# Kernel tuning notes

Measured on AMD Instinct MI355X. Metric: run time of the kernel, lower is better.

## Reference

```python
import jax, jax.numpy as jnp
import numpy as np

B, S, D, H, HD = 4, 2048, 768, 12, 64


def setup_inputs() -> dict:
    key = jax.random.key(0)
    ks = jax.random.split(key, 9)
    s = 1.0 / np.sqrt(D)
    return {
        "hidden_state": jax.random.normal(ks[0], (B, S, D), jnp.float32),
        "Wq": jax.random.normal(ks[1], (H, D, HD), jnp.float32) * s,
        "bq": jax.random.normal(ks[2], (H, HD), jnp.float32) * 0.02,
        "Wk": jax.random.normal(ks[3], (H, D, HD), jnp.float32) * s,
        "bk": jax.random.normal(ks[4], (H, HD), jnp.float32) * 0.02,
        "Wv": jax.random.normal(ks[5], (H, D, HD), jnp.float32) * s,
        "bv": jax.random.normal(ks[6], (H, HD), jnp.float32) * 0.02,
        "Wo": jax.random.normal(ks[7], (D, D), jnp.float32) * s,
        "bo": jax.random.normal(ks[8], (D,), jnp.float32) * 0.02,
    }


def reference(hidden_state, Wq, bq, Wk, bk, Wv, bv, Wo, bo):
    # per-head projections, batched over heads: [B,H,S,HD]
    q = jnp.einsum("bsd,hde->bhse", hidden_state, Wq) + bq[None, :, None, :]
    k = jnp.einsum("bsd,hde->bhse", hidden_state, Wk) + bk[None, :, None, :]
    v = jnp.einsum("bsd,hde->bhse", hidden_state, Wv) + bv[None, :, None, :]
    scale = 1.0 / jnp.sqrt(jnp.asarray(HD, q.dtype))
    scores = jnp.einsum("bhse,bhte->bhst", q, k) * scale  # [B,H,S,S]
    attn = jax.nn.softmax(scores, axis=-1)
    out = jnp.einsum("bhst,bhte->bhse", attn, v)  # [B,H,S,HD]
    # concat heads in head order -> [B,S,D]
    out = out.transpose(0, 2, 1, 3).reshape(B, S, D)
    return out @ Wo.T + bo
```

## Files before the change

### kernel.cpp

```cpp
#include <hip/hip_runtime.h>
#include <hip/hip_bf16.h>

typedef unsigned short u16;
typedef __attribute__((ext_vector_type(8))) short short8;
typedef __attribute__((ext_vector_type(4))) float f32x4;

#define B_ 4
#define S_ 2048
#define D_ 768
#define H_ 12
#define HD_ 64

__device__ __forceinline__ u16 f2bf(float f) {
  union { float f; unsigned u; } c; c.f = f;
  unsigned u = c.u;
  unsigned lsb = (u >> 16) & 1u;
  u += 0x7fffu + lsb;
  return (u16)(u >> 16);
}

__global__ __launch_bounds__(256) void k_cvt_x(const float* __restrict__ x,
                                               u16* __restrict__ xb, int n4) {
  int i = blockIdx.x * 256 + threadIdx.x;
  if (i < n4) {
    float4 v = reinterpret_cast<const float4*>(x)[i];
    ushort4 o;
    o.x = f2bf(v.x); o.y = f2bf(v.y); o.z = f2bf(v.z); o.w = f2bf(v.w);
    reinterpret_cast<ushort4*>(xb)[i] = o;
  }
}

__global__ __launch_bounds__(256) void k_repack_w(const float* __restrict__ Wq,
                                                  const float* __restrict__ Wk,
                                                  const float* __restrict__ Wv,
                                                  const float* __restrict__ Wo,
                                                  u16* __restrict__ Wt,
                                                  u16* __restrict__ Wob) {
  int idx = blockIdx.x * 256 + threadIdx.x;
  const int WSZ = D_ * D_;
  if (idx < 3 * WSZ) {
    int t = idx / WSZ, r = idx % WSZ;
    int n = r / D_, d = r % D_;
    int h = n >> 6, e = n & 63;
    const float* W = (t == 0) ? Wq : (t == 1) ? Wk : Wv;
    Wt[idx] = f2bf(W[h * (D_ * HD_) + d * HD_ + e]);
  } else {
    int o = idx - 3 * WSZ;
    if (o < WSZ) Wob[o] = f2bf(Wo[o]);
  }
}

__global__ __launch_bounds__(256) void k_gemm_qkv(const u16* __restrict__ Xb,
                                                  const u16* __restrict__ Wt,
                                                  const float* __restrict__ bq,
                                                  const float* __restrict__ bk,
                                                  u16* __restrict__ Qw,
                                                  u16* __restrict__ Kw) {
  const int t = blockIdx.z;
  const u16* Bmat = Wt + t * (D_ * D_);
  const float* bias = (t == 0) ? bq : bk;
  u16* Out = (t == 0) ? Qw : Kw;
  const float scale = (t == 0) ? 0.125f : 1.0f;
  const int m0 = blockIdx.x * 128, n0 = blockIdx.y * 128;
  __shared__ __align__(16) u16 Al[128][40];
  __shared__ __align__(16) u16 Bl[128][40];
  const int tid = threadIdx.x;
  const int lane = tid & 63, w = tid >> 6;
  const int wm = (w >> 1) * 64, wn = (w & 1) * 64;
  const int lg = lane >> 4, lr = lane & 15;
  f32x4 acc[4][4] = {};
  for (int k0 = 0; k0 < D_; k0 += 32) {
    __syncthreads();
#pragma unroll
    for (int rep = 0; rep < 2; ++rep) {
      int item = tid + rep * 256;
      int row = item >> 2, ch = (item & 3) * 8;
      uint4 av = *reinterpret_cast<const uint4*>(&Xb[(m0 + row) * D_ + k0 + ch]);
      *reinterpret_cast<uint4*>(&Al[row][ch]) = av;
      uint4 bv2 = *reinterpret_cast<const uint4*>(&Bmat[(n0 + row) * D_ + k0 + ch]);
      *reinterpret_cast<uint4*>(&Bl[row][ch]) = bv2;
    }
    __syncthreads();
    short8 af[4], bf[4];
#pragma unroll
    for (int i = 0; i < 4; i++)
      af[i] = *reinterpret_cast<const short8*>(&Al[wm + i * 16 + lr][lg * 8]);
#pragma unroll
    for (int i = 0; i < 4; i++)
      bf[i] = *reinterpret_cast<const short8*>(&Bl[wn + i * 16 + lr][lg * 8]);
#pragma unroll
    for (int mi = 0; mi < 4; mi++)
#pragma unroll
      for (int ni = 0; ni < 4; ni++)
        acc[mi][ni] = __builtin_amdgcn_mfma_f32_16x16x32_bf16(af[mi], bf[ni], acc[mi][ni], 0, 0, 0);
  }
#pragma unroll
  for (int ni = 0; ni < 4; ni++) {
    int n = n0 + wn + ni * 16 + lr;
    float bn = bias[n];
    int h = n >> 6, e = n & 63;
#pragma unroll
    for (int mi = 0; mi < 4; mi++) {
#pragma unroll
      for (int r = 0; r < 4; r++) {
        int m = m0 + wm + mi * 16 + lg * 4 + r;
        int b = m >> 11, s = m & 2047;
        float v = (acc[mi][ni][r] + bn) * scale;
        Out[((b * H_ + h) * S_ + s) * HD_ + e] = f2bf(v);
      }
    }
  }
}

__global__ __launch_bounds__(256) void k_gemm_v(const u16* __restrict__ Xb,
                                                const u16* __restrict__ Wt,
                                                const float* __restrict__ bv,
                                                u16* __restrict__ VwT) {
  const u16* Bmat = Wt + 2 * (D_ * D_);
  const int m0 = blockIdx.x * 128, n0 = blockIdx.y * 128;
  __shared__ __align__(16) u16 Al[128][40];
  __shared__ __align__(16) u16 Bl[128][40];
  const int tid = threadIdx.x;
  const int lane = tid & 63, w = tid >> 6;
  const int wm = (w >> 1) * 64, wn = (w & 1) * 64;
  const int lg = lane >> 4, lr = lane & 15;
  f32x4 acc[4][4] = {};
  for (int k0 = 0; k0 < D_; k0 += 32) {
    __syncthreads();
#pragma unroll
    for (int rep = 0; rep < 2; ++rep) {
      int item = tid + rep * 256;
      int row = item >> 2, ch = (item & 3) * 8;
      uint4 av = *reinterpret_cast<const uint4*>(&Xb[(m0 + row) * D_ + k0 + ch]);
      *reinterpret_cast<uint4*>(&Al[row][ch]) = av;
      uint4 bv2 = *reinterpret_cast<const uint4*>(&Bmat[(n0 + row) * D_ + k0 + ch]);
      *reinterpret_cast<uint4*>(&Bl[row][ch]) = bv2;
    }
    __syncthreads();
    short8 af[4], bf[4];
#pragma unroll
    for (int i = 0; i < 4; i++)
      af[i] = *reinterpret_cast<const short8*>(&Al[wm + i * 16 + lr][lg * 8]);
#pragma unroll
    for (int i = 0; i < 4; i++)
      bf[i] = *reinterpret_cast<const short8*>(&Bl[wn + i * 16 + lr][lg * 8]);
#pragma unroll
    for (int ni = 0; ni < 4; ni++)
#pragma unroll
      for (int mi = 0; mi < 4; mi++)
        acc[ni][mi] = __builtin_amdgcn_mfma_f32_16x16x32_bf16(bf[ni], af[mi], acc[ni][mi], 0, 0, 0);
  }
#pragma unroll
  for (int ni = 0; ni < 4; ni++) {
#pragma unroll
    for (int r = 0; r < 4; r++) {
      int n = n0 + wn + ni * 16 + lg * 4 + r;
      int h = n >> 6, e = n & 63;
      float bn = bv[n];
#pragma unroll
      for (int mi = 0; mi < 4; mi++) {
        int m = m0 + wm + mi * 16 + lr;
        int b = m >> 11, s = m & 2047;
        VwT[((b * H_ + h) * HD_ + e) * S_ + s] = f2bf(acc[ni][mi][r] + bn);
      }
    }
  }
}

__global__ __launch_bounds__(256) void k_attn(const u16* __restrict__ Qw,
                                              const u16* __restrict__ Kw,
                                              const u16* __restrict__ VwT,
                                              u16* __restrict__ An) {
  const int qb = blockIdx.x;
  const int bh = blockIdx.y;
  const int b = bh / H_, h = bh % H_;
  const int tid = threadIdx.x, lane = tid & 63, w = tid >> 6;
  const int lg = lane >> 4, lr = lane & 15;
  __shared__ __align__(16) u16 Kl[64][72];
  __shared__ __align__(16) u16 Vt[64][72];
  __shared__ __align__(16) u16 Pb[4][32][72];
  const u16* Qp = Qw + (bh * S_ + qb * 128 + w * 32) * HD_;
  const u16* Kp = Kw + bh * S_ * HD_;
  const u16* VTp = VwT + bh * HD_ * S_;
  const int srow0 = tid >> 3, srow1 = (tid + 256) >> 3;
  const int sch = (tid & 7) * 8;
  short8 qf[2][2];
#pragma unroll
  for (int qif = 0; qif < 2; qif++)
#pragma unroll
    for (int es = 0; es < 2; es++)
      qf[qif][es] = *reinterpret_cast<const short8*>(&Qp[(qif * 16 + lr) * HD_ + es * 32 + lg * 8]);
  f32x4 acc[2][4] = {};
  float mcol[2] = {-INFINITY, -INFINITY};
  float lcol[2] = {0.f, 0.f};

  {
    uint4 k0a = *reinterpret_cast<const uint4*>(&Kp[srow0 * HD_ + sch]);
    uint4 k0b = *reinterpret_cast<const uint4*>(&Kp[srow1 * HD_ + sch]);
    uint4 v0a = *reinterpret_cast<const uint4*>(&VTp[srow0 * S_ + sch]);
    uint4 v0b = *reinterpret_cast<const uint4*>(&VTp[srow1 * S_ + sch]);
    *reinterpret_cast<uint4*>(&Kl[srow0][sch]) = k0a;
    *reinterpret_cast<uint4*>(&Kl[srow1][sch]) = k0b;
    *reinterpret_cast<uint4*>(&Vt[srow0][sch]) = v0a;
    *reinterpret_cast<uint4*>(&Vt[srow1][sch]) = v0b;
  }
  __syncthreads();

  for (int t0 = 0; t0 < S_; t0 += 64) {
    const int tn = t0 + 64;
    uint4 kna, knb, vna, vnb;
    if (tn < S_) {
      kna = *reinterpret_cast<const uint4*>(&Kp[(tn + srow0) * HD_ + sch]);
      knb = *reinterpret_cast<const uint4*>(&Kp[(tn + srow1) * HD_ + sch]);
      vna = *reinterpret_cast<const uint4*>(&VTp[srow0 * S_ + tn + sch]);
      vnb = *reinterpret_cast<const uint4*>(&VTp[srow1 * S_ + tn + sch]);
    }
    f32x4 st[4][2] = {};
#pragma unroll
    for (int es = 0; es < 2; es++) {
      short8 kf[4];
#pragma unroll
      for (int kjf = 0; kjf < 4; kjf++)
        kf[kjf] = *reinterpret_cast<const short8*>(&Kl[kjf * 16 + lr][es * 32 + lg * 8]);
      __builtin_amdgcn_s_setprio(1);
#pragma unroll
      for (int kjf = 0; kjf < 4; kjf++)
#pragma unroll
        for (int qif = 0; qif < 2; qif++)
          st[kjf][qif] = __builtin_amdgcn_mfma_f32_16x16x32_bf16(kf[kjf], qf[qif][es], st[kjf][qif], 0, 0, 0);
      __builtin_amdgcn_s_setprio(0);
    }
#pragma unroll
    for (int qif = 0; qif < 2; qif++) {
      float tmax = st[0][qif][0];
#pragma unroll
      for (int kjf = 0; kjf < 4; kjf++)
#pragma unroll
        for (int r = 0; r < 4; r++) tmax = fmaxf(tmax, st[kjf][qif][r]);
      tmax = fmaxf(tmax, __shfl_xor(tmax, 16));
      tmax = fmaxf(tmax, __shfl_xor(tmax, 32));
      float mnew = fmaxf(mcol[qif], tmax);
      float csc = __expf(mcol[qif] - mnew);
      float tsum = 0.f;
      u16 pk[4][4];
#pragma unroll
      for (int kjf = 0; kjf < 4; kjf++) {
#pragma unroll
        for (int r = 0; r < 4; r++) {
          float p = __expf(st[kjf][qif][r] - mnew);
          tsum += p;
          pk[kjf][r] = f2bf(p);
        }
      }
      tsum += __shfl_xor(tsum, 16);
      tsum += __shfl_xor(tsum, 32);
      lcol[qif] = lcol[qif] * csc + tsum;
      mcol[qif] = mnew;
#pragma unroll
      for (int kjf = 0; kjf < 4; kjf++) {
        ushort4 pv;
        pv.x = pk[kjf][0]; pv.y = pk[kjf][1]; pv.z = pk[kjf][2]; pv.w = pk[kjf][3];
        *reinterpret_cast<ushort4*>(&Pb[w][qif * 16 + lr][kjf * 16 + lg * 4]) = pv;
      }
#pragma unroll
      for (int r = 0; r < 4; r++) {
        float f = __shfl(csc, lg * 4 + r);
#pragma unroll
        for (int ef = 0; ef < 4; ef++) acc[qif][ef][r] *= f;
      }
    }
#pragma unroll
    for (int ks = 0; ks < 2; ks++) {
      short8 pa[2];
#pragma unroll
      for (int qif = 0; qif < 2; qif++)
        pa[qif] = *reinterpret_cast<const short8*>(&Pb[w][qif * 16 + lr][ks * 32 + lg * 8]);
      __builtin_amdgcn_s_setprio(1);
#pragma unroll
      for (int ef = 0; ef < 4; ef++) {
        short8 vf = *reinterpret_cast<const short8*>(&Vt[ef * 16 + lr][ks * 32 + lg * 8]);
#pragma unroll
        for (int qif = 0; qif < 2; qif++)
          acc[qif][ef] = __builtin_amdgcn_mfma_f32_16x16x32_bf16(pa[qif], vf, acc[qif][ef], 0, 0, 0);
      }
      __builtin_amdgcn_s_setprio(0);
    }
    __syncthreads();
    if (tn < S_) {
      *reinterpret_cast<uint4*>(&Kl[srow0][sch]) = kna;
      *reinterpret_cast<uint4*>(&Kl[srow1][sch]) = knb;
      *reinterpret_cast<uint4*>(&Vt[srow0][sch]) = vna;
      *reinterpret_cast<uint4*>(&Vt[srow1][sch]) = vnb;
    }
    __syncthreads();
  }
  int qbase = qb * 128 + w * 32;
#pragma unroll
  for (int qif = 0; qif < 2; qif++) {
#pragma unroll
    for (int r = 0; r < 4; r++) {
      float lv = __shfl(lcol[qif], lg * 4 + r);
      float linv = 1.0f / lv;
      int s = qbase + qif * 16 + lg * 4 + r;
      u16* op = &An[(b * S_ + s) * D_ + h * HD_];
#pragma unroll
      for (int ef = 0; ef < 4; ef++) op[ef * 16 + lr] = f2bf(acc[qif][ef][r] * linv);
    }
  }
}

__global__ __launch_bounds__(256) void k_gemm_out(const u16* __restrict__ An,
                                                  const u16* __restrict__ Wob,
                                                  const float* __restrict__ bo,
                                                  float* __restrict__ out) {
  const int m0 = blockIdx.x * 128, n0 = blockIdx.y * 128;
  __shared__ __align__(16) u16 Al[128][40];
  __shared__ __align__(16) u16 Bl[128][40];
  const int tid = threadIdx.x;
  const int lane = tid & 63, w = tid >> 6;
  const int wm = (w >> 1) * 64, wn = (w & 1) * 64;
  const int lg = lane >> 4, lr = lane & 15;
  f32x4 acc[4][4] = {};
  for (int k0 = 0; k0 < D_; k0 += 32) {
    __syncthreads();
#pragma unroll
    for (int rep = 0; rep < 2; ++rep) {
      int item = tid + rep * 256;
      int row = item >> 2, ch = (item & 3) * 8;
      uint4 av = *reinterpret_cast<const uint4*>(&An[(m0 + row) * D_ + k0 + ch]);
      *reinterpret_cast<uint4*>(&Al[row][ch]) = av;
      uint4 bv2 = *reinterpret_cast<const uint4*>(&Wob[(n0 + row) * D_ + k0 + ch]);
      *reinterpret_cast<uint4*>(&Bl[row][ch]) = bv2;
    }
    __syncthreads();
    short8 af[4], bf[4];
#pragma unroll
    for (int i = 0; i < 4; i++)
      af[i] = *reinterpret_cast<const short8*>(&Al[wm + i * 16 + lr][lg * 8]);
#pragma unroll
    for (int i = 0; i < 4; i++)
      bf[i] = *reinterpret_cast<const short8*>(&Bl[wn + i * 16 + lr][lg * 8]);
#pragma unroll
    for (int mi = 0; mi < 4; mi++)
#pragma unroll
      for (int ni = 0; ni < 4; ni++)
        acc[mi][ni] = __builtin_amdgcn_mfma_f32_16x16x32_bf16(af[mi], bf[ni], acc[mi][ni], 0, 0, 0);
  }
#pragma unroll
  for (int ni = 0; ni < 4; ni++) {
    int n = n0 + wn + ni * 16 + lr;
    float bn = bo[n];
#pragma unroll
    for (int mi = 0; mi < 4; mi++) {
#pragma unroll
      for (int r = 0; r < 4; r++) {
        int m = m0 + wm + mi * 16 + lg * 4 + r;
        out[m * D_ + n] = acc[mi][ni][r] + bn;
      }
    }
  }
}

extern "C" void kernel_launch(void* const* d_in, const int* in_sizes, int n_in,
                              void* d_out, int out_size, void* d_ws, size_t ws_size,
                              hipStream_t stream) {
  const float* X  = (const float*)d_in[0];
  const float* Wq = (const float*)d_in[1];
  const float* bq = (const float*)d_in[2];
  const float* Wk = (const float*)d_in[3];
  const float* bk = (const float*)d_in[4];
  const float* Wv = (const float*)d_in[5];
  const float* bv = (const float*)d_in[6];
  const float* Wo = (const float*)d_in[7];
  const float* bo = (const float*)d_in[8];
  float* out = (float*)d_out;

  char* ws = (char*)d_ws;
  u16* Xb  = (u16*)(ws + 0);
  u16* Wt  = (u16*)(ws + 12582912);
  u16* Wob = (u16*)(ws + 16121856);
  u16* Qw  = (u16*)(ws + 17301504);
  u16* Kw  = (u16*)(ws + 29884416);
  u16* VwT = (u16*)(ws + 42467328);
  u16* An  = (u16*)(ws + 55050240);

  const int nx4 = (B_ * S_ * D_) / 4;
  k_cvt_x<<<dim3(nx4 / 256), dim3(256), 0, stream>>>(X, Xb, nx4);
  k_repack_w<<<dim3((4 * D_ * D_) / 256), dim3(256), 0, stream>>>(Wq, Wk, Wv, Wo, Wt, Wob);
  k_gemm_qkv<<<dim3(64, 6, 2), dim3(256), 0, stream>>>(Xb, Wt, bq, bk, Qw, Kw);
  k_gemm_v<<<dim3(64, 6), dim3(256), 0, stream>>>(Xb, Wt, bv, VwT);
  k_attn<<<dim3(16, 48), dim3(256), 0, stream>>>(Qw, Kw, VwT, An);
  k_gemm_out<<<dim3(64, 6), dim3(256), 0, stream>>>(An, Wob, bo, out);
}
```

Baseline: 316.5 us.

## Prefetch GEMM tiles, use exp2 lazy-rescale softmax, packed bf16 conversions, tiled weight repack

Each GEMM now loads the next K-slice into registers while the MFMAs for the current slice run, so global-load latency overlaps with compute. The attention softmax switches to exp2 by folding log2(e) into the Q scale, and only rescales the running max and accumulator when the new max exceeds the old one by more than 10. Float-to-bf16 conversions use the hardware v_cvt_pk_bf16_f32 instruction instead of software rounding. The weight repack is split into an LDS-tiled transpose for Wq/Wk/Wv and a plain vectorized conversion for Wo. The changes trade an extra barrier per K step and higher register use for lower latency and fewer ALU instructions, and the lazy rescale relies on bounded growth of the exponent for numerical safety.

```diff
diff --git a/kernel.cpp b/kernel.cpp
--- a/kernel.cpp
+++ b/kernel.cpp
@@ -19,34 +19,47 @@
   return (u16)(u >> 16);
 }
 
+__device__ __forceinline__ unsigned cvt_pk(float lo, float hi) {
+  unsigned r;
+  asm("v_cvt_pk_bf16_f32 %0, %1, %2" : "=v"(r) : "v"(lo), "v"(hi));
+  return r;
+}
+
 __global__ __launch_bounds__(256) void k_cvt_x(const float* __restrict__ x,
                                                u16* __restrict__ xb, int n4) {
   int i = blockIdx.x * 256 + threadIdx.x;
   if (i < n4) {
     float4 v = reinterpret_cast<const float4*>(x)[i];
     ushort4 o;
-    o.x = f2bf(v.x); o.y = f2bf(v.y); o.z = f2bf(v.z); o.w = f2bf(v.w);
+    unsigned c01 = cvt_pk(v.x, v.y), c23 = cvt_pk(v.z, v.w);
+    o.x = (u16)c01; o.y = (u16)(c01 >> 16); o.z = (u16)c23; o.w = (u16)(c23 >> 16);
     reinterpret_cast<ushort4*>(xb)[i] = o;
   }
 }
 
-__global__ __launch_bounds__(256) void k_repack_w(const float* __restrict__ Wq,
-                                                  const float* __restrict__ Wk,
-                                                  const float* __restrict__ Wv,
-                                                  const float* __restrict__ Wo,
-                                                  u16* __restrict__ Wt,
-                                                  u16* __restrict__ Wob) {
-  int idx = blockIdx.x * 256 + threadIdx.x;
-  const int WSZ = D_ * D_;
-  if (idx < 3 * WSZ) {
-    int t = idx / WSZ, r = idx % WSZ;
-    int n = r / D_, d = r % D_;
-    int h = n >> 6, e = n & 63;
-    const float* W = (t == 0) ? Wq : (t == 1) ? Wk : Wv;
-    Wt[idx] = f2bf(W[h * (D_ * HD_) + d * HD_ + e]);
-  } else {
-    int o = idx - 3 * WSZ;
-    if (o < WSZ) Wob[o] = f2bf(Wo[o]);
+__global__ __launch_bounds__(256) void k_repack_qkv(const float* __restrict__ Wq,
+                                                    const float* __restrict__ Wk,
+                                                    const float* __restrict__ Wv,
+                                                    u16* __restrict__ Wt) {
+  const int h = blockIdx.x;
+  const int d0 = blockIdx.y * 64;
+  const int t = blockIdx.z;
+  const float* W = (t == 0) ? Wq : (t == 1) ? Wk : Wv;
+  const int tid = threadIdx.x;
+  __shared__ __align__(16) u16 T[64][72];
+#pragma unroll
+  for (int i = 0; i < 16; i++) {
+    int item = i * 256 + tid;
+    int dl = item >> 6, e = item & 63;
+    T[e][dl] = f2bf(W[h * (D_ * HD_) + (d0 + dl) * HD_ + e]);
+  }
+  __syncthreads();
+#pragma unroll
+  for (int i = 0; i < 4; i++) {
+    int item = i * 256 + tid;
+    int e = item >> 4, dl4 = (item & 15) * 4;
+    ushort4 o = *reinterpret_cast<const ushort4*>(&T[e][dl4]);
+    *reinterpret_cast<ushort4*>(&Wt[t * (D_ * D_) + (h * 64 + e) * D_ + d0 + dl4]) = o;
   }
 }
 
@@ -60,7 +73,7 @@
   const u16* Bmat = Wt + t * (D_ * D_);
   const float* bias = (t == 0) ? bq : bk;
   u16* Out = (t == 0) ? Qw : Kw;
-  const float scale = (t == 0) ? 0.125f : 1.0f;
+  const float scale = (t == 0) ? 0.18033688f : 1.0f;
   const int m0 = blockIdx.x * 128, n0 = blockIdx.y * 128;
   __shared__ __align__(16) u16 Al[128][40];
   __shared__ __align__(16) u16 Bl[128][40];
@@ -68,19 +81,27 @@
   const int lane = tid & 63, w = tid >> 6;
   const int wm = (w >> 1) * 64, wn = (w & 1) * 64;
   const int lg = lane >> 4, lr = lane & 15;
+  const int sr0 = tid >> 2, sr1 = (tid + 256) >> 2;
+  const int sc = (tid & 3) * 8;
+  uint4 pa0, pa1, pb0, pb1;
+  auto ld = [&](int k0) {
+    pa0 = *reinterpret_cast<const uint4*>(&Xb[(m0 + sr0) * D_ + k0 + sc]);
+    pa1 = *reinterpret_cast<const uint4*>(&Xb[(m0 + sr1) * D_ + k0 + sc]);
+    pb0 = *reinterpret_cast<const uint4*>(&Bmat[(n0 + sr0) * D_ + k0 + sc]);
+    pb1 = *reinterpret_cast<const uint4*>(&Bmat[(n0 + sr1) * D_ + k0 + sc]);
+  };
+  auto st_lds = [&]() {
+    *reinterpret_cast<uint4*>(&Al[sr0][sc]) = pa0;
+    *reinterpret_cast<uint4*>(&Al[sr1][sc]) = pa1;
+    *reinterpret_cast<uint4*>(&Bl[sr0][sc]) = pb0;
+    *reinterpret_cast<uint4*>(&Bl[sr1][sc]) = pb1;
+  };
   f32x4 acc[4][4] = {};
+  ld(0); st_lds();
+  __syncthreads();
   for (int k0 = 0; k0 < D_; k0 += 32) {
-    __syncthreads();
-#pragma unroll
-    for (int rep = 0; rep < 2; ++rep) {
-      int item = tid + rep * 256;
-      int row = item >> 2, ch = (item & 3) * 8;
-      uint4 av = *reinterpret_cast<const uint4*>(&Xb[(m0 + row) * D_ + k0 + ch]);
-      *reinterpret_cast<uint4*>(&Al[row][ch]) = av;
-      uint4 bv2 = *reinterpret_cast<const uint4*>(&Bmat[(n0 + row) * D_ + k0 + ch]);
-      *reinterpret_cast<uint4*>(&Bl[row][ch]) = bv2;
-    }
-    __syncthreads();
+    bool more = (k0 + 32) < D_;
+    if (more) ld(k0 + 32);
     short8 af[4], bf[4];
 #pragma unroll
     for (int i = 0; i < 4; i++)
@@ -93,21 +114,31 @@
 #pragma unroll
       for (int ni = 0; ni < 4; ni++)
         acc[mi][ni] = __builtin_amdgcn_mfma_f32_16x16x32_bf16(af[mi], bf[ni], acc[mi][ni], 0, 0, 0);
+    if (more) {
+      __syncthreads();
+      st_lds();
+      __syncthreads();
+    }
   }
 #pragma unroll
   for (int ni = 0; ni < 4; ni++) {
     int n = n0 + wn + ni * 16 + lr;
-    float bn = bias[n];
+    float bns = bias[n] * scale;
     int h = n >> 6, e = n & 63;
 #pragma unroll
     for (int mi = 0; mi < 4; mi++) {
-#pragma unroll
-      for (int r = 0; r < 4; r++) {
-        int m = m0 + wm + mi * 16 + lg * 4 + r;
-        int b = m >> 11, s = m & 2047;
-        float v = (acc[mi][ni][r] + bn) * scale;
-        Out[((b * H_ + h) * S_ + s) * HD_ + e] = f2bf(v);
-      }
+      float v0 = fmaf(acc[mi][ni][0], scale, bns);
+      float v1 = fmaf(acc[mi][ni][1], scale, bns);
+      float v2 = fmaf(acc[mi][ni][2], scale, bns);
+      float v3 = fmaf(acc[mi][ni][3], scale, bns);
+      unsigned c01 = cvt_pk(v0, v1), c23 = cvt_pk(v2, v3);
+      int m = m0 + wm + mi * 16 + lg * 4;
+      int b = m >> 11, s = m & 2047;
+      u16* base = &Out[((b * H_ + h) * S_ + s) * HD_ + e];
+      base[0]       = (u16)c01;
+      base[HD_]     = (u16)(c01 >> 16);
+      base[2 * HD_] = (u16)c23;
+      base[3 * HD_] = (u16)(c23 >> 16);
     }
   }
 }
@@ -124,19 +155,27 @@
   const int lane = tid & 63, w = tid >> 6;
   const int wm = (w >> 1) * 64, wn = (w & 1) * 64;
   const int lg = lane >> 4, lr = lane & 15;
+  const int sr0 = tid >> 2, sr1 = (tid + 256) >> 2;
+  const int sc = (tid & 3) * 8;
+  uint4 pa0, pa1, pb0, pb1;
+  auto ld = [&](int k0) {
+    pa0 = *reinterpret_cast<const uint4*>(&Xb[(m0 + sr0) * D_ + k0 + sc]);
+    pa1 = *reinterpret_cast<const uint4*>(&Xb[(m0 + sr1) * D_ + k0 + sc]);
+    pb0 = *reinterpret_cast<const uint4*>(&Bmat[(n0 + sr0) * D_ + k0 + sc]);
+    pb1 = *reinterpret_cast<const uint4*>(&Bmat[(n0 + sr1) * D_ + k0 + sc]);
+  };
+  auto st_lds = [&]() {
+    *reinterpret_cast<uint4*>(&Al[sr0][sc]) = pa0;
+    *reinterpret_cast<uint4*>(&Al[sr1][sc]) = pa1;
+    *reinterpret_cast<uint4*>(&Bl[sr0][sc]) = pb0;
+    *reinterpret_cast<uint4*>(&Bl[sr1][sc]) = pb1;
+  };
   f32x4 acc[4][4] = {};
+  ld(0); st_lds();
+  __syncthreads();
   for (int k0 = 0; k0 < D_; k0 += 32) {
-    __syncthreads();
-#pragma unroll
-    for (int rep = 0; rep < 2; ++rep) {
-      int item = tid + rep * 256;
-      int row = item >> 2, ch = (item & 3) * 8;
-      uint4 av = *reinterpret_cast<const uint4*>(&Xb[(m0 + row) * D_ + k0 + ch]);
-      *reinterpret_cast<uint4*>(&Al[row][ch]) = av;
-      uint4 bv2 = *reinterpret_cast<const uint4*>(&Bmat[(n0 + row) * D_ + k0 + ch]);
-      *reinterpret_cast<uint4*>(&Bl[row][ch]) = bv2;
-    }
-    __syncthreads();
+    bool more = (k0 + 32) < D_;
+    if (more) ld(k0 + 32);
     short8 af[4], bf[4];
 #pragma unroll
     for (int i = 0; i < 4; i++)
@@ -149,6 +188,11 @@
 #pragma unroll
       for (int mi = 0; mi < 4; mi++)
         acc[ni][mi] = __builtin_amdgcn_mfma_f32_16x16x32_bf16(bf[ni], af[mi], acc[ni][mi], 0, 0, 0);
+    if (more) {
+      __syncthreads();
+      st_lds();
+      __syncthreads();
+    }
   }
 #pragma unroll
   for (int ni = 0; ni < 4; ni++) {
@@ -157,12 +201,16 @@
       int n = n0 + wn + ni * 16 + lg * 4 + r;
       int h = n >> 6, e = n & 63;
       float bn = bv[n];
-#pragma unroll
-      for (int mi = 0; mi < 4; mi++) {
-        int m = m0 + wm + mi * 16 + lr;
-        int b = m >> 11, s = m & 2047;
-        VwT[((b * H_ + h) * HD_ + e) * S_ + s] = f2bf(acc[ni][mi][r] + bn);
-      }
+      float v0 = acc[ni][0][r] + bn, v1 = acc[ni][1][r] + bn;
+      float v2 = acc[ni][2][r] + bn, v3 = acc[ni][3][r] + bn;
+      unsigned c01 = cvt_pk(v0, v1), c23 = cvt_pk(v2, v3);
+      int m = m0 + wm + lr;
+      int b = m >> 11, s = m & 2047;
+      u16* base = &VwT[((b * H_ + h) * HD_ + e) * S_ + s];
+      base[0]  = (u16)c01;
+      base[16] = (u16)(c01 >> 16);
+      base[32] = (u16)c23;
+      base[48] = (u16)(c23 >> 16);
     }
   }
 }
@@ -239,35 +287,35 @@
         for (int r = 0; r < 4; r++) tmax = fmaxf(tmax, st[kjf][qif][r]);
       tmax = fmaxf(tmax, __shfl_xor(tmax, 16));
       tmax = fmaxf(tmax, __shfl_xor(tmax, 32));
-      float mnew = fmaxf(mcol[qif], tmax);
-      float csc = __expf(mcol[qif] - mnew);
+      if (__any(tmax > mcol[qif] + 10.0f)) {
+        float mnew = fmaxf(mcol[qif], tmax);
+        float csc = exp2f(mcol[qif] - mnew);
+        mcol[qif] = mnew;
+        lcol[qif] *= csc;
+#pragma unroll
+        for (int r = 0; r < 4; r++) {
+          float f = __shfl(csc, lg * 4 + r);
+#pragma unroll
+          for (int ef = 0; ef < 4; ef++) acc[qif][ef][r] *= f;
+        }
+      }
+      float m = mcol[qif];
       float tsum = 0.f;
-      u16 pk[4][4];
 #pragma unroll
       for (int kjf = 0; kjf < 4; kjf++) {
-#pragma unroll
-        for (int r = 0; r < 4; r++) {
-          float p = __expf(st[kjf][qif][r] - mnew);
-          tsum += p;
-          pk[kjf][r] = f2bf(p);
-        }
+        float p0 = exp2f(st[kjf][qif][0] - m);
+        float p1 = exp2f(st[kjf][qif][1] - m);
+        float p2 = exp2f(st[kjf][qif][2] - m);
+        float p3 = exp2f(st[kjf][qif][3] - m);
+        tsum += (p0 + p1) + (p2 + p3);
+        uint2 pv;
+        pv.x = cvt_pk(p0, p1);
+        pv.y = cvt_pk(p2, p3);
+        *reinterpret_cast<uint2*>(&Pb[w][qif * 16 + lr][kjf * 16 + lg * 4]) = pv;
       }
       tsum += __shfl_xor(tsum, 16);
       tsum += __shfl_xor(tsum, 32);
-      lcol[qif] = lcol[qif] * csc + tsum;
-      mcol[qif] = mnew;
-#pragma unroll
-      for (int kjf = 0; kjf < 4; kjf++) {
-        ushort4 pv;
-        pv.x = pk[kjf][0]; pv.y = pk[kjf][1]; pv.z = pk[kjf][2]; pv.w = pk[kjf][3];
-        *reinterpret_cast<ushort4*>(&Pb[w][qif * 16 + lr][kjf * 16 + lg * 4]) = pv;
-      }
-#pragma unroll
-      for (int r = 0; r < 4; r++) {
-        float f = __shfl(csc, lg * 4 + r);
-#pragma unroll
-        for (int ef = 0; ef < 4; ef++) acc[qif][ef][r] *= f;
-      }
+      lcol[qif] += tsum;
     }
 #pragma unroll
     for (int ks = 0; ks < 2; ks++) {
@@ -303,8 +351,13 @@
       float linv = 1.0f / lv;
       int s = qbase + qif * 16 + lg * 4 + r;
       u16* op = &An[(b * S_ + s) * D_ + h * HD_];
-#pragma unroll
-      for (int ef = 0; ef < 4; ef++) op[ef * 16 + lr] = f2bf(acc[qif][ef][r] * linv);
+      float a0 = acc[qif][0][r] * linv, a1 = acc[qif][1][r] * linv;
+      float a2 = acc[qif][2][r] * linv, a3 = acc[qif][3][r] * linv;
+      unsigned c01 = cvt_pk(a0, a1), c23 = cvt_pk(a2, a3);
+      op[0 * 16 + lr] = (u16)c01;
+      op[1 * 16 + lr] = (u16)(c01 >> 16);
+      op[2 * 16 + lr] = (u16)c23;
+      op[3 * 16 + lr] = (u16)(c23 >> 16);
     }
   }
 }
@@ -320,19 +373,27 @@
   const int lane = tid & 63, w = tid >> 6;
   const int wm = (w >> 1) * 64, wn = (w & 1) * 64;
   const int lg = lane >> 4, lr = lane & 15;
+  const int sr0 = tid >> 2, sr1 = (tid + 256) >> 2;
+  const int sc = (tid & 3) * 8;
+  uint4 pa0, pa1, pb0, pb1;
+  auto ld = [&](int k0) {
+    pa0 = *reinterpret_cast<const uint4*>(&An[(m0 + sr0) * D_ + k0 + sc]);
+    pa1 = *reinterpret_cast<const uint4*>(&An[(m0 + sr1) * D_ + k0 + sc]);
+    pb0 = *reinterpret_cast<const uint4*>(&Wob[(n0 + sr0) * D_ + k0 + sc]);
+    pb1 = *reinterpret_cast<const uint4*>(&Wob[(n0 + sr1) * D_ + k0 + sc]);
+  };
+  auto st_lds = [&]() {
+    *reinterpret_cast<uint4*>(&Al[sr0][sc]) = pa0;
+    *reinterpret_cast<uint4*>(&Al[sr1][sc]) = pa1;
+    *reinterpret_cast<uint4*>(&Bl[sr0][sc]) = pb0;
+    *reinterpret_cast<uint4*>(&Bl[sr1][sc]) = pb1;
+  };
   f32x4 acc[4][4] = {};
+  ld(0); st_lds();
+  __syncthreads();
   for (int k0 = 0; k0 < D_; k0 += 32) {
-    __syncthreads();
-#pragma unroll
-    for (int rep = 0; rep < 2; ++rep) {
-      int item = tid + rep * 256;
-      int row = item >> 2, ch = (item & 3) * 8;
-      uint4 av = *reinterpret_cast<const uint4*>(&An[(m0 + row) * D_ + k0 + ch]);
-      *reinterpret_cast<uint4*>(&Al[row][ch]) = av;
-      uint4 bv2 = *reinterpret_cast<const uint4*>(&Wob[(n0 + row) * D_ + k0 + ch]);
-      *reinterpret_cast<uint4*>(&Bl[row][ch]) = bv2;
-    }
-    __syncthreads();
+    bool more = (k0 + 32) < D_;
+    if (more) ld(k0 + 32);
     short8 af[4], bf[4];
 #pragma unroll
     for (int i = 0; i < 4; i++)
@@ -345,6 +406,11 @@
 #pragma unroll
       for (int ni = 0; ni < 4; ni++)
         acc[mi][ni] = __builtin_amdgcn_mfma_f32_16x16x32_bf16(af[mi], bf[ni], acc[mi][ni], 0, 0, 0);
+    if (more) {
+      __syncthreads();
+      st_lds();
+      __syncthreads();
+    }
   }
 #pragma unroll
   for (int ni = 0; ni < 4; ni++) {
@@ -385,8 +451,10 @@
   u16* An  = (u16*)(ws + 55050240);
 
   const int nx4 = (B_ * S_ * D_) / 4;
+  const int nw4 = (D_ * D_) / 4;
   k_cvt_x<<<dim3(nx4 / 256), dim3(256), 0, stream>>>(X, Xb, nx4);
-  k_repack_w<<<dim3((4 * D_ * D_) / 256), dim3(256), 0, stream>>>(Wq, Wk, Wv, Wo, Wt, Wob);
+  k_cvt_x<<<dim3(nw4 / 256), dim3(256), 0, stream>>>(Wo, Wob, nw4);
+  k_repack_qkv<<<dim3(12, 12, 3), dim3(256), 0, stream>>>(Wq, Wk, Wv, Wt);
   k_gemm_qkv<<<dim3(64, 6, 2), dim3(256), 0, stream>>>(Xb, Wt, bq, bk, Qw, Kw);
   k_gemm_v<<<dim3(64, 6), dim3(256), 0, stream>>>(Xb, Wt, bv, VwT);
   k_attn<<<dim3(16, 48), dim3(256), 0, stream>>>(Qw, Kw, VwT, An);
```

Measured after the change: 297.0 us. 6.2% less time.
